# Kernel optimization log

Measured on AMD Instinct MI355X. Metric: run time of the kernel, lower is better.

## Reference

```python
import jax, jax.numpy as jnp
import numpy as np
from jax import lax

TAU = 2.0
NUM_HEADS = 8
EPS = 1e-5
ALPHA = 4.0  # surrogate sigmoid sharpness

@jax.custom_vjp
def heaviside(x):
    # torch.heaviside(x, 1.0): 1 for x >= 0 (value 1 at x==0), 0 for x < 0
    return (x >= 0).astype(x.dtype)

def _hv_fwd(x):
    return (x >= 0).astype(x.dtype), x

def _hv_bwd(x, g):
    s = jax.nn.sigmoid(x * ALPHA)
    return (g * s * (1.0 - s) * ALPHA,)

heaviside.defvjp(_hv_fwd, _hv_bwd)

def lif(x):
    # Leaky-integrate-fire recurrence over leading time axis. x: [T, ...]
    def step(v, xt):
        v = v + (xt - v) / TAU                 # leakage
        s = heaviside(v - 1.0)                 # fire (v_threshold = 1.0)
        v = (1.0 - lax.stop_gradient(s)) * v   # hard reset (detached spike)
        return v, s
    _, spikes = lax.scan(step, jnp.zeros_like(x[0]), x)
    return spikes

def conv1x1(x, w):
    # x: [T,B,Cin,H,W], w: [Cout,Cin] (1x1 conv, no bias)
    return jnp.einsum('tbchw,dc->tbdhw', x, w)

def bn(x, gamma, beta, mean, var):
    # BatchNorm2d in eval mode (running stats), per-channel over axis 2
    shp = (1, 1, -1, 1, 1)
    inv = gamma.reshape(shp) / jnp.sqrt(var.reshape(shp) + EPS)
    return (x - mean.reshape(shp)) * inv + beta.reshape(shp)

def setup_inputs():
    key = jax.random.key(0)
    ks = jax.random.split(key, 10)
    T, B, C, H, W = 4, 32, 256, 16, 16
    Cv = C  # lamda_ratio = 1

    def w_init(k, o, i):
        return jax.random.normal(k, (o, i), jnp.float32) * (1.0 / np.sqrt(i))

    def bn_params(k, c):
        k1, k2, k3, k4 = jax.random.split(k, 4)
        gamma = jax.random.uniform(k1, (c,), jnp.float32, 0.5, 1.5)
        beta = jax.random.normal(k2, (c,), jnp.float32) * 0.1
        mean = jax.random.normal(k3, (c,), jnp.float32) * 0.1
        var = jax.random.uniform(k4, (c,), jnp.float32, 0.5, 1.5)
        return gamma, beta, mean, var

    x = jax.random.normal(ks[0], (T, B, C, H, W), jnp.float32)
    q_w = w_init(ks[1], C, C)
    k_w = w_init(ks[2], C, C)
    v_w = w_init(ks[3], Cv, C)
    proj_w = w_init(ks[4], C, Cv)
    q_gamma, q_beta, q_mean, q_var = bn_params(ks[5], C)
    k_gamma, k_beta, k_mean, k_var = bn_params(ks[6], C)
    v_gamma, v_beta, v_mean, v_var = bn_params(ks[7], Cv)
    p_gamma, p_beta, p_mean, p_var = bn_params(ks[8], C)
    return {
        'x': x,
        'q_w': q_w, 'q_gamma': q_gamma, 'q_beta': q_beta, 'q_mean': q_mean, 'q_var': q_var,
        'k_w': k_w, 'k_gamma': k_gamma, 'k_beta': k_beta, 'k_mean': k_mean, 'k_var': k_var,
        'v_w': v_w, 'v_gamma': v_gamma, 'v_beta': v_beta, 'v_mean': v_mean, 'v_var': v_var,
        'proj_w': proj_w, 'p_gamma': p_gamma, 'p_beta': p_beta, 'p_mean': p_mean, 'p_var': p_var,
    }

def reference(x, q_w, q_gamma, q_beta, q_mean, q_var,
              k_w, k_gamma, k_beta, k_mean, k_var,
              v_w, v_gamma, v_beta, v_mean, v_var,
              proj_w, p_gamma, p_beta, p_mean, p_var):
    T, B, C, H, W = x.shape
    N = H * W
    Cv = v_w.shape[0]
    hd = C // NUM_HEADS
    hdv = Cv // NUM_HEADS
    scale = (C // NUM_HEADS) ** -0.5

    xs = lif(x)  # head_spike

    q = lif(bn(conv1x1(xs, q_w), q_gamma, q_beta, q_mean, q_var))  # [T,B,C,H,W] binary
    k = lif(bn(conv1x1(xs, k_w), k_gamma, k_beta, k_mean, k_var))
    v = lif(bn(conv1x1(xs, v_w), v_gamma, v_beta, v_mean, v_var))  # [T,B,Cv,H,W]

    # channel c = h*hd + d; flatten spatial -> tokens N, split heads
    q = q.reshape(T, B, NUM_HEADS, hd, N).transpose(0, 1, 2, 4, 3)   # [T,B,h,N,d]
    k = k.reshape(T, B, NUM_HEADS, hd, N).transpose(0, 1, 2, 4, 3)
    v = v.reshape(T, B, NUM_HEADS, hdv, N).transpose(0, 1, 2, 4, 3)  # [T,B,h,N,dv]

    attn = jnp.einsum('tbhnd,tbhmd->tbhnm', q, k)                    # QK^T
    out = jnp.einsum('tbhnm,tbhmd->tbhnd', attn, v) * (scale * 2.0)  # (QK^T)V * 2*scale

    out = out.transpose(0, 1, 2, 4, 3).reshape(T, B, Cv, N)          # [T,B,Cv,N]
    out = lif(out)                                                   # attn_spike
    out = out.reshape(T, B, Cv, H, W)
    out = bn(conv1x1(out, proj_w), p_gamma, p_beta, p_mean, p_var)   # [T,B,C,H,W]
    return out
```

## Files before the change

### kernel.cpp

```cpp
#include <hip/hip_runtime.h>

#define TT 4
#define BB 32
#define CC 256
#define NN 256
#define EPSf 1e-5f
#define MULTf 0.35355339059327373f
#define MARGINf 1e-3f
#define FLAG_CAP 524288u

typedef __attribute__((ext_vector_type(8))) short s16x8;
typedef __attribute__((ext_vector_type(4))) float f32x4;
typedef unsigned char uchar;
typedef unsigned int uint;
typedef unsigned short ushort;

__device__ __forceinline__ ushort f2bf_rn(float f) {
  uint u = __float_as_uint(f);
  u = (u + 0x7FFFu + ((u >> 16) & 1u)) >> 16;
  return (ushort)u;
}
__device__ __forceinline__ float bf2f(ushort b) {
  return __uint_as_float(((uint)b) << 16);
}

__device__ __forceinline__ void gload_lds16(const void* g, void* l) {
  __builtin_amdgcn_global_load_lds(
      (const __attribute__((address_space(1))) uint*)g,
      (__attribute__((address_space(3))) uint*)l, 16, 0, 0);
}

__global__ __launch_bounds__(256) void k_lif_frag(const float* __restrict__ x,
                                                  uchar* __restrict__ xsF,
                                                  uchar* __restrict__ xsP) {
#pragma clang fp contract(off)
  const int tid = threadIdx.x;
  const int nt = blockIdx.x;
  const int ks = blockIdx.y;
  const int b = blockIdx.z;
  const int nl = tid & 63;
  const int oct = tid >> 6;
  const int n = nt * 64 + nl;
  const int c0 = ks * 32 + oct * 8;
  const size_t stride = (size_t)BB * CC * NN;
  const float* xb = x + ((size_t)b * CC + c0) * NN + n;

  float v[8];
#pragma unroll
  for (int j = 0; j < 8; ++j) v[j] = 0.f;

#pragma unroll
  for (int t = 0; t < TT; ++t) {
    ushort sp[8];
    uint pm = 0;
#pragma unroll
    for (int j = 0; j < 8; ++j) {
      float xt = xb[t * stride + (size_t)j * NN];
      float d = (xt - v[j]) * 0.5f;
      v[j] = v[j] + d;
      bool s = (v[j] >= 1.0f);
      sp[j] = s ? (ushort)0x3F80 : (ushort)0;
      if (s) { v[j] = 0.f; pm |= 1u << j; }
    }
    uint4* dst = reinterpret_cast<uint4*>(xsF) +
                 (((size_t)(t * BB + b) * 16 + (n >> 4)) * 512 + ks * 64 + oct * 16 + (n & 15));
    uint4 o;
    o.x = (uint)sp[0] | ((uint)sp[1] << 16);
    o.y = (uint)sp[2] | ((uint)sp[3] << 16);
    o.z = (uint)sp[4] | ((uint)sp[5] << 16);
    o.w = (uint)sp[6] | ((uint)sp[7] << 16);
    *dst = o;
    xsP[(((size_t)(t * BB + b) * NN + n) << 5) + ks * 4 + oct] = (uchar)pm;
  }
}

__global__ __launch_bounds__(256) void k_prep_w(
    const float* __restrict__ qw, const float* __restrict__ kw,
    const float* __restrict__ vw, const float* __restrict__ pw,
    uchar* __restrict__ wfq, uchar* __restrict__ wfp,
    uint* __restrict__ flags) {
  const int gid = blockIdx.x * 256 + threadIdx.x;
  if (gid < 4) flags[gid] = 0;
  const int ob2 = gid >> 9;
  const int e = gid & 511;
  const int ks = e >> 6, l = e & 63;
  const float* W;
  uchar* outb;
  int ob_out, nob;
  if (ob2 < 48) {
    const int sel = ob2 >> 4;
    W = sel == 0 ? qw : (sel == 1 ? kw : vw);
    W += ((size_t)((ob2 & 15) * 16 + (l & 15))) * CC;
    outb = wfq; ob_out = ob2; nob = 48;
  } else {
    W = pw + ((size_t)((ob2 - 48) * 16 + (l & 15))) * CC;
    outb = wfp; ob_out = ob2 - 48; nob = 16;
  }
  const int c0 = ks * 32 + (l >> 4) * 8;
  float wv[8];
  *reinterpret_cast<float4*>(&wv[0]) = *reinterpret_cast<const float4*>(W + c0);
  *reinterpret_cast<float4*>(&wv[4]) = *reinterpret_cast<const float4*>(W + c0 + 4);
  ushort hi[8], lo[8];
#pragma unroll
  for (int j = 0; j < 8; ++j) {
    hi[j] = f2bf_rn(wv[j]);
    lo[j] = f2bf_rn(wv[j] - bf2f(hi[j]));
  }
  const size_t base = (((size_t)ob_out * 8 + ks) * 64 + l) * 16;
  const size_t sstr = (size_t)nob * 8 * 64 * 16;
  *reinterpret_cast<uint4*>(outb + base) = *reinterpret_cast<const uint4*>(hi);
  *reinterpret_cast<uint4*>(outb + sstr + base) = *reinterpret_cast<const uint4*>(lo);
}

__global__ __launch_bounds__(256, 2) void k_qkv_mfma(
    const uchar* __restrict__ xsF, const uchar* __restrict__ wfq,
    const float* __restrict__ qga, const float* __restrict__ qbe, const float* __restrict__ qme, const float* __restrict__ qva,
    const float* __restrict__ kga, const float* __restrict__ kbe, const float* __restrict__ kme, const float* __restrict__ kva,
    const float* __restrict__ vga, const float* __restrict__ vbe, const float* __restrict__ vme, const float* __restrict__ vva,
    ushort* __restrict__ qp, uint* __restrict__ flags) {
  __shared__ short lsB[2][4][8][64][8];
  const int tid = threadIdx.x;
  const int w = tid >> 6, lane = tid & 63;
  const int lhi = lane >> 4, llo = lane & 15;
  const int wr = w >> 1, wc = w & 1;
  const int oc0 = blockIdx.x * 64;
  const int ntile = blockIdx.y;
  const int b = blockIdx.z;
  const int sel = oc0 >> 8;
  const float* G  = sel == 0 ? qga : (sel == 1 ? kga : vga);
  const float* Be = sel == 0 ? qbe : (sel == 1 ? kbe : vbe);
  const float* Mn = sel == 0 ? qme : (sel == 1 ? kme : vme);
  const float* Vr = sel == 0 ? qva : (sel == 1 ? kva : vva);

  s16x8 wfr[2][2][8];
#pragma unroll
  for (int s = 0; s < 2; ++s)
#pragma unroll
    for (int mf = 0; mf < 2; ++mf) {
      const int ob = blockIdx.x * 4 + wr * 2 + mf;
#pragma unroll
      for (int ks = 0; ks < 8; ++ks)
        wfr[s][mf][ks] = *reinterpret_cast<const s16x8*>(
            wfq + ((((size_t)s * 48 + ob) * 8 + ks) * 64 + lane) * 16);
    }

  float inv8[2][4], mean8[2][4], beta8[2][4];
#pragma unroll
  for (int mf = 0; mf < 2; ++mf)
#pragma unroll
    for (int r = 0; r < 4; ++r) {
      const int ocb = (oc0 & 255) + wr * 32 + mf * 16 + lhi * 4 + r;
      inv8[mf][r] = G[ocb] / sqrtf(Vr[ocb] + EPSf);
      mean8[mf][r] = Mn[ocb];
      beta8[mf][r] = Be[ocb];
    }

  auto STAGE = [&](int buf, int t) {
    const uchar* src = xsF + (((size_t)(t * BB + b) * 16 + ntile * 4) * 8192);
#pragma unroll
    for (int k2 = 0; k2 < 8; ++k2) {
      const int chunk = w * 8 + k2;
      gload_lds16(src + (size_t)chunk * 1024 + lane * 16,
                  reinterpret_cast<char*>(&lsB[buf][0][0][0][0]) + chunk * 1024);
    }
  };

  float vst[2][2][4];
#pragma unroll
  for (int mf = 0; mf < 2; ++mf)
#pragma unroll
    for (int nf = 0; nf < 2; ++nf)
#pragma unroll
      for (int r = 0; r < 4; ++r) vst[mf][nf][r] = 0.f;
  uint fl = 0;
  ushort qm[TT][4];

  STAGE(0, 0);
  __syncthreads();

#pragma unroll
  for (int t = 0; t < TT; ++t) {
    const int cur = t & 1;
    if (t + 1 < TT) STAGE(cur ^ 1, t + 1);

    f32x4 acc[2][2];
#pragma unroll
    for (int mf = 0; mf < 2; ++mf)
#pragma unroll
      for (int nf = 0; nf < 2; ++nf) acc[mf][nf] = (f32x4){0.f, 0.f, 0.f, 0.f};

#pragma unroll
    for (int ks = 0; ks < 8; ++ks) {
      s16x8 b0 = *reinterpret_cast<const s16x8*>(&lsB[cur][wc * 2][ks][lane][0]);
      s16x8 b1 = *reinterpret_cast<const s16x8*>(&lsB[cur][wc * 2 + 1][ks][lane][0]);
#pragma unroll
      for (int s = 0; s < 2; ++s)
#pragma unroll
        for (int mf = 0; mf < 2; ++mf) {
          acc[mf][0] = __builtin_amdgcn_mfma_f32_16x16x32_bf16(wfr[s][mf][ks], b0, acc[mf][0], 0, 0, 0);
          acc[mf][1] = __builtin_amdgcn_mfma_f32_16x16x32_bf16(wfr[s][mf][ks], b1, acc[mf][1], 0, 0, 0);
        }
    }

#pragma unroll
    for (int mf = 0; mf < 2; ++mf)
#pragma unroll
      for (int nf = 0; nf < 2; ++nf)
#pragma unroll
        for (int r = 0; r < 4; ++r) {
          float y = (acc[mf][nf][r] - mean8[mf][r]) * inv8[mf][r] + beta8[mf][r];
          float v = vst[mf][nf][r];
          v = v + (y - v) * 0.5f;
          const bool sp = (v >= 1.0f);
          if (fabsf(v - 1.0f) < MARGINf) fl |= 1u << ((mf * 2 + nf) * 4 + r);
          const unsigned long long m = __ballot(sp);
          if (llo == r) qm[t][mf * 2 + nf] = (ushort)((m >> (lhi * 16)) & 0xFFFFull);
          vst[mf][nf][r] = sp ? 0.f : v;
        }
    __syncthreads();
  }

  if (llo < 4) {
#pragma unroll
    for (int t = 0; t < TT; ++t) {
      ushort* qrow = qp + (size_t)(t * BB + b) * 768 * 16;
#pragma unroll
      for (int mf = 0; mf < 2; ++mf)
#pragma unroll
        for (int nf = 0; nf < 2; ++nf) {
          const int oc = oc0 + wr * 32 + mf * 16 + lhi * 4 + llo;
          qrow[(size_t)oc * 16 + ntile * 4 + wc * 2 + nf] = qm[t][mf * 2 + nf];
        }
    }
  }

  if (fl) {
    const int cnt = __popc(fl);
    uint base = atomicAdd(flags, (uint)cnt);
#pragma unroll
    for (int mf = 0; mf < 2; ++mf)
#pragma unroll
      for (int nf = 0; nf < 2; ++nf)
#pragma unroll
        for (int r = 0; r < 4; ++r)
          if (fl & (1u << ((mf * 2 + nf) * 4 + r))) {
            const int oc = oc0 + wr * 32 + mf * 16 + lhi * 4 + r;
            const int n = ntile * 64 + wc * 32 + nf * 16 + llo;
            if (base < FLAG_CAP) flags[4 + base] = (((uint)(b << 10) | (uint)oc) << 8) | (uint)n;
            base++;
          }
  }
}

__global__ __launch_bounds__(256) void k_fix(
    const uchar* __restrict__ xsP,
    const float* __restrict__ qw, const float* __restrict__ kw, const float* __restrict__ vw,
    const float* __restrict__ qga, const float* __restrict__ qbe, const float* __restrict__ qme, const float* __restrict__ qva,
    const float* __restrict__ kga, const float* __restrict__ kbe, const float* __restrict__ kme, const float* __restrict__ kva,
    const float* __restrict__ vga, const float* __restrict__ vbe, const float* __restrict__ vme, const float* __restrict__ vva,
    uint* __restrict__ qp32, const uint* __restrict__ flags) {
#pragma clang fp contract(off)
  const uint cnt = min(flags[0], FLAG_CAP);
  for (uint i = blockIdx.x * 256 + threadIdx.x; i < cnt; i += gridDim.x * 256) {
    const uint e = flags[4 + i];
    const int n = e & 255;
    const int oc = (e >> 8) & 1023;
    const int b = e >> 18;
    const int sel = oc >> 8, ocl = oc & 255;
    const float* W = (sel == 0 ? qw : (sel == 1 ? kw : vw)) + (size_t)ocl * CC;
    const float* G  = sel == 0 ? qga : (sel == 1 ? kga : vga);
    const float* Be = sel == 0 ? qbe : (sel == 1 ? kbe : vbe);
    const float* Mn = sel == 0 ? qme : (sel == 1 ? kme : vme);
    const float* Vr = sel == 0 ? qva : (sel == 1 ? kva : vva);

    uint bw[4][8];
#pragma unroll
    for (int t = 0; t < TT; ++t) {
      const uint4* p = reinterpret_cast<const uint4*>(
          xsP + (((size_t)(t * BB + b) * NN + n) << 5));
      uint4 a = p[0], c4 = p[1];
      bw[t][0] = a.x;  bw[t][1] = a.y;  bw[t][2] = a.z;  bw[t][3] = a.w;
      bw[t][4] = c4.x; bw[t][5] = c4.y; bw[t][6] = c4.z; bw[t][7] = c4.w;
    }

    const float4* W4 = reinterpret_cast<const float4*>(W);
    float a0 = 0.f, a1 = 0.f, a2 = 0.f, a3 = 0.f;
#pragma unroll
    for (int g = 0; g < 32; ++g) {
      const float4 w0 = W4[2 * g];
      const float4 w1 = W4[2 * g + 1];
      const uint s0 = bw[0][g >> 2] >> ((g & 3) * 8);
      const uint s1 = bw[1][g >> 2] >> ((g & 3) * 8);
      const uint s2 = bw[2][g >> 2] >> ((g & 3) * 8);
      const uint s3 = bw[3][g >> 2] >> ((g & 3) * 8);
      const float wv[8] = {w0.x, w0.y, w0.z, w0.w, w1.x, w1.y, w1.z, w1.w};
#pragma unroll
      for (int j = 0; j < 8; ++j) {
        a0 = fmaf(wv[j], (float)((s0 >> j) & 1u), a0);
        a1 = fmaf(wv[j], (float)((s1 >> j) & 1u), a1);
        a2 = fmaf(wv[j], (float)((s2 >> j) & 1u), a2);
        a3 = fmaf(wv[j], (float)((s3 >> j) & 1u), a3);
      }
    }
    float accs[4] = {a0, a1, a2, a3};

    const float inv = G[ocl] / sqrtf(Vr[ocl] + EPSf);
    const float mean = Mn[ocl], beta = Be[ocl];
    float v = 0.f;
#pragma unroll
    for (int t = 0; t < TT; ++t) {
      float xm = accs[t] - mean;
      float y = xm * inv;
      y = y + beta;
      float d = (y - v) * 0.5f;
      v = v + d;
      const bool sp = (v >= 1.0f);
      const size_t widx = ((size_t)(t * BB + b) * 768 + oc) * 8 + (n >> 5);
      const uint bit = 1u << (n & 31);
      if (sp) atomicOr(&qp32[widx], bit);
      else atomicAnd(&qp32[widx], ~bit);
      if (sp) v = 0.f;
    }
  }
}

__global__ __launch_bounds__(1024) void k_attn(const ushort* __restrict__ qp,
                                               uchar* __restrict__ attnF) {
  __shared__ uint Qb[32][8], Kb[32][8], Vb[32][8];
  __shared__ int KtV[32][32];
  const int tid = threadIdx.x;
  const int b = blockIdx.x >> 3;
  const int h = blockIdx.x & 7;
  const int n = tid & 255;
  const int jg = tid >> 8;
  const int wordn = n >> 5, bitn = n & 31;

  float vst[8];
#pragma unroll
  for (int j = 0; j < 8; ++j) vst[j] = 0.f;

  for (int t = 0; t < TT; ++t) {
    __syncthreads();
    const ushort* base = qp + (size_t)(t * BB + b) * 768 * 16;
    if (tid < 768) {
      const int arr = tid >> 8;
      const int idx = tid & 255;
      const int ch = idx >> 3, wv2 = idx & 7;
      const uint val = *reinterpret_cast<const uint*>(
          base + (size_t)(arr * 256 + h * 32 + ch) * 16 + wv2 * 2);
      uint(*dst)[8] = (arr == 0) ? Qb : (arr == 1) ? Kb : Vb;
      dst[ch][wv2] = val;
    }
    __syncthreads();
    {
      const int ii = tid >> 5, jj = tid & 31;
      int s = 0;
#pragma unroll
      for (int w8 = 0; w8 < 8; ++w8) s += __popc(Kb[ii][w8] & Vb[jj][w8]);
      KtV[ii][jj] = s;
    }
    __syncthreads();
    int acc[8];
#pragma unroll
    for (int j = 0; j < 8; ++j) acc[j] = 0;
#pragma unroll 4
    for (int ii = 0; ii < 32; ++ii) {
      const int qb = (int)((Qb[ii][wordn] >> bitn) & 1u);
      const int4 k0 = *reinterpret_cast<const int4*>(&KtV[ii][jg * 8]);
      const int4 k1 = *reinterpret_cast<const int4*>(&KtV[ii][jg * 8 + 4]);
      acc[0] += k0.x * qb; acc[1] += k0.y * qb;
      acc[2] += k0.z * qb; acc[3] += k0.w * qb;
      acc[4] += k1.x * qb; acc[5] += k1.y * qb;
      acc[6] += k1.z * qb; acc[7] += k1.w * qb;
    }
    ushort sbit[8];
    {
#pragma clang fp contract(off)
#pragma unroll
      for (int j = 0; j < 8; ++j) {
        float y = (float)acc[j] * MULTf;
        float v = vst[j];
        float d = (y - v) * 0.5f;
        v = v + d;
        const bool sp = (v >= 1.0f);
        sbit[j] = sp ? (ushort)0x3F80 : (ushort)0;
        vst[j] = sp ? 0.f : v;
      }
    }
    uint4 o;
    o.x = (uint)sbit[0] | ((uint)sbit[1] << 16);
    o.y = (uint)sbit[2] | ((uint)sbit[3] << 16);
    o.z = (uint)sbit[4] | ((uint)sbit[5] << 16);
    o.w = (uint)sbit[6] | ((uint)sbit[7] << 16);
    uint4* dst4 = reinterpret_cast<uint4*>(attnF) +
                  (((size_t)(t * BB + b) * 16 + (n >> 4)) * 512 + h * 64 + jg * 16 + (n & 15));
    *dst4 = o;
  }
}

__global__ __launch_bounds__(256, 2) void k_proj_mfma(
    const uchar* __restrict__ attnF, const uchar* __restrict__ wfp,
    const float* __restrict__ pga, const float* __restrict__ pbe,
    const float* __restrict__ pme, const float* __restrict__ pva,
    float* __restrict__ out) {
  __shared__ short lsB[4][8][64][8];
  const int tid = threadIdx.x;
  const int w = tid >> 6, lane = tid & 63;
  const int lhi = lane >> 4, llo = lane & 15;
  const int wr = w >> 1, wc = w & 1;
  const int oc0 = blockIdx.x * 64;
  const int ntile = blockIdx.y;
  const int tb = blockIdx.z;

  s16x8 wfr[2][2][8];
#pragma unroll
  for (int s = 0; s < 2; ++s)
#pragma unroll
    for (int mf = 0; mf < 2; ++mf) {
      const int ob = blockIdx.x * 4 + wr * 2 + mf;
#pragma unroll
      for (int ks = 0; ks < 8; ++ks)
        wfr[s][mf][ks] = *reinterpret_cast<const s16x8*>(
            wfp + ((((size_t)s * 16 + ob) * 8 + ks) * 64 + lane) * 16);
    }

  float inv8[2][4], mean8[2][4], beta8[2][4];
#pragma unroll
  for (int mf = 0; mf < 2; ++mf)
#pragma unroll
    for (int r = 0; r < 4; ++r) {
      const int ocb = oc0 + wr * 32 + mf * 16 + lhi * 4 + r;
      inv8[mf][r] = pga[ocb] / sqrtf(pva[ocb] + EPSf);
      mean8[mf][r] = pme[ocb];
      beta8[mf][r] = pbe[ocb];
    }

  const uchar* src = attnF + (((size_t)tb * 16 + ntile * 4) * 8192);
#pragma unroll
  for (int k2 = 0; k2 < 8; ++k2) {
    const int chunk = w * 8 + k2;
    gload_lds16(src + (size_t)chunk * 1024 + lane * 16,
                reinterpret_cast<char*>(&lsB[0][0][0][0]) + chunk * 1024);
  }
  __syncthreads();

  f32x4 acc[2][2];
#pragma unroll
  for (int mf = 0; mf < 2; ++mf)
#pragma unroll
    for (int nf = 0; nf < 2; ++nf) acc[mf][nf] = (f32x4){0.f, 0.f, 0.f, 0.f};

#pragma unroll
  for (int ks = 0; ks < 8; ++ks) {
    s16x8 b0 = *reinterpret_cast<const s16x8*>(&lsB[wc * 2][ks][lane][0]);
    s16x8 b1 = *reinterpret_cast<const s16x8*>(&lsB[wc * 2 + 1][ks][lane][0]);
#pragma unroll
    for (int s = 0; s < 2; ++s)
#pragma unroll
      for (int mf = 0; mf < 2; ++mf) {
        acc[mf][0] = __builtin_amdgcn_mfma_f32_16x16x32_bf16(wfr[s][mf][ks], b0, acc[mf][0], 0, 0, 0);
        acc[mf][1] = __builtin_amdgcn_mfma_f32_16x16x32_bf16(wfr[s][mf][ks], b1, acc[mf][1], 0, 0, 0);
      }
  }

#pragma unroll
  for (int mf = 0; mf < 2; ++mf)
#pragma unroll
    for (int nf = 0; nf < 2; ++nf)
#pragma unroll
      for (int r = 0; r < 4; ++r) {
        const int oc = oc0 + wr * 32 + mf * 16 + lhi * 4 + r;
        const int nn = ntile * 64 + wc * 32 + nf * 16 + llo;
        float y = (acc[mf][nf][r] - mean8[mf][r]) * inv8[mf][r] + beta8[mf][r];
        out[((size_t)tb * CC + oc) * NN + nn] = y;
      }
}

extern "C" void kernel_launch(void* const* d_in, const int* in_sizes, int n_in,
                              void* d_out, int out_size, void* d_ws, size_t ws_size,
                              hipStream_t stream) {
  const float* x = (const float*)d_in[0];
  const float* q_w = (const float*)d_in[1];
  const float* q_g = (const float*)d_in[2];
  const float* q_b = (const float*)d_in[3];
  const float* q_m = (const float*)d_in[4];
  const float* q_v = (const float*)d_in[5];
  const float* k_w = (const float*)d_in[6];
  const float* k_g = (const float*)d_in[7];
  const float* k_b = (const float*)d_in[8];
  const float* k_m = (const float*)d_in[9];
  const float* k_v = (const float*)d_in[10];
  const float* v_w = (const float*)d_in[11];
  const float* v_g = (const float*)d_in[12];
  const float* v_b = (const float*)d_in[13];
  const float* v_m = (const float*)d_in[14];
  const float* v_v = (const float*)d_in[15];
  const float* p_w = (const float*)d_in[16];
  const float* p_g = (const float*)d_in[17];
  const float* p_b = (const float*)d_in[18];
  const float* p_m = (const float*)d_in[19];
  const float* p_v = (const float*)d_in[20];

  uchar* ws = (uchar*)d_ws;
  uchar* xsF  = ws;
  ushort* qp  = (ushort*)(ws + 16777216);
  uchar* wfq  = ws + 19922944;
  uchar* wfp  = ws + 20709376;
  uint* flags = (uint*)(ws + 20971520);
  uchar* xsP  = ws + 23068672;

  k_prep_w<<<dim3(128), 256, 0, stream>>>(q_w, k_w, v_w, p_w, wfq, wfp, flags);
  k_lif_frag<<<dim3(4, 8, 32), 256, 0, stream>>>(x, xsF, xsP);
  k_qkv_mfma<<<dim3(12, 4, 32), 256, 0, stream>>>(xsF, wfq,
                                                  q_g, q_b, q_m, q_v,
                                                  k_g, k_b, k_m, k_v,
                                                  v_g, v_b, v_m, v_v,
                                                  qp, flags);
  k_fix<<<dim3(64), 256, 0, stream>>>(xsP, q_w, k_w, v_w,
                                      q_g, q_b, q_m, q_v,
                                      k_g, k_b, k_m, k_v,
                                      v_g, v_b, v_m, v_v,
                                      (uint*)qp, flags);
  k_attn<<<dim3(256), 1024, 0, stream>>>(qp, xsF );
  k_proj_mfma<<<dim3(4, 4, 128), 256, 0, stream>>>(xsF, wfp, p_g, p_b, p_m, p_v,
                                                   (float*)d_out);
}
```

Before: 114.1 us.

## Merge front kernels, swap QKV operand staging, and remap blocks across XCDs

```diff
diff --git a/kernel.cpp b/kernel.cpp
--- a/kernel.cpp
+++ b/kernel.cpp
@@ -30,140 +30,129 @@
       (__attribute__((address_space(3))) uint*)l, 16, 0, 0);
 }
 
-__global__ __launch_bounds__(256) void k_lif_frag(const float* __restrict__ x,
-                                                  uchar* __restrict__ xsF,
-                                                  uchar* __restrict__ xsP) {
-#pragma clang fp contract(off)
-  const int tid = threadIdx.x;
-  const int nt = blockIdx.x;
-  const int ks = blockIdx.y;
-  const int b = blockIdx.z;
-  const int nl = tid & 63;
-  const int oct = tid >> 6;
-  const int n = nt * 64 + nl;
-  const int c0 = ks * 32 + oct * 8;
-  const size_t stride = (size_t)BB * CC * NN;
-  const float* xb = x + ((size_t)b * CC + c0) * NN + n;
-
-  float v[8];
-#pragma unroll
-  for (int j = 0; j < 8; ++j) v[j] = 0.f;
-
-#pragma unroll
-  for (int t = 0; t < TT; ++t) {
-    ushort sp[8];
-    uint pm = 0;
-#pragma unroll
-    for (int j = 0; j < 8; ++j) {
-      float xt = xb[t * stride + (size_t)j * NN];
-      float d = (xt - v[j]) * 0.5f;
-      v[j] = v[j] + d;
-      bool s = (v[j] >= 1.0f);
-      sp[j] = s ? (ushort)0x3F80 : (ushort)0;
-      if (s) { v[j] = 0.f; pm |= 1u << j; }
-    }
-    uint4* dst = reinterpret_cast<uint4*>(xsF) +
-                 (((size_t)(t * BB + b) * 16 + (n >> 4)) * 512 + ks * 64 + oct * 16 + (n & 15));
-    uint4 o;
-    o.x = (uint)sp[0] | ((uint)sp[1] << 16);
-    o.y = (uint)sp[2] | ((uint)sp[3] << 16);
-    o.z = (uint)sp[4] | ((uint)sp[5] << 16);
-    o.w = (uint)sp[6] | ((uint)sp[7] << 16);
-    *dst = o;
-    xsP[(((size_t)(t * BB + b) * NN + n) << 5) + ks * 4 + oct] = (uchar)pm;
-  }
-}
-
-__global__ __launch_bounds__(256) void k_prep_w(
+__global__ __launch_bounds__(256) void k_front(
+    const float* __restrict__ x, uchar* __restrict__ xsF, uchar* __restrict__ xsP,
     const float* __restrict__ qw, const float* __restrict__ kw,
     const float* __restrict__ vw, const float* __restrict__ pw,
-    uchar* __restrict__ wfq, uchar* __restrict__ wfp,
-    uint* __restrict__ flags) {
-  const int gid = blockIdx.x * 256 + threadIdx.x;
-  if (gid < 4) flags[gid] = 0;
-  const int ob2 = gid >> 9;
-  const int e = gid & 511;
-  const int ks = e >> 6, l = e & 63;
-  const float* W;
-  uchar* outb;
-  int ob_out, nob;
-  if (ob2 < 48) {
-    const int sel = ob2 >> 4;
-    W = sel == 0 ? qw : (sel == 1 ? kw : vw);
-    W += ((size_t)((ob2 & 15) * 16 + (l & 15))) * CC;
-    outb = wfq; ob_out = ob2; nob = 48;
+    uchar* __restrict__ wfq, uchar* __restrict__ wfp, uint* __restrict__ flags) {
+  const int tid = threadIdx.x;
+  const int bid = blockIdx.x;
+  if (bid < 1024) {
+#pragma clang fp contract(off)
+    const int nt = bid & 3;
+    const int ks = (bid >> 2) & 7;
+    const int b = bid >> 5;
+    const int nl = tid & 63;
+    const int oct = tid >> 6;
+    const int n = nt * 64 + nl;
+    const int c0 = ks * 32 + oct * 8;
+    const size_t stride = (size_t)BB * CC * NN;
+    const float* xb = x + ((size_t)b * CC + c0) * NN + n;
+
+    float v[8];
+#pragma unroll
+    for (int j = 0; j < 8; ++j) v[j] = 0.f;
+
+#pragma unroll
+    for (int t = 0; t < TT; ++t) {
+      ushort sp[8];
+      uint pm = 0;
+#pragma unroll
+      for (int j = 0; j < 8; ++j) {
+        float xt = xb[t * stride + (size_t)j * NN];
+        float d = (xt - v[j]) * 0.5f;
+        v[j] = v[j] + d;
+        bool s = (v[j] >= 1.0f);
+        sp[j] = s ? (ushort)0x3F80 : (ushort)0;
+        if (s) { v[j] = 0.f; pm |= 1u << j; }
+      }
+      uint4* dst = reinterpret_cast<uint4*>(xsF) +
+                   (((size_t)(t * BB + b) * 16 + (n >> 4)) * 512 + ks * 64 + oct * 16 + (n & 15));
+      uint4 o;
+      o.x = (uint)sp[0] | ((uint)sp[1] << 16);
+      o.y = (uint)sp[2] | ((uint)sp[3] << 16);
+      o.z = (uint)sp[4] | ((uint)sp[5] << 16);
+      o.w = (uint)sp[6] | ((uint)sp[7] << 16);
+      *dst = o;
+      xsP[(((size_t)(t * BB + b) * NN + n) << 5) + ks * 4 + oct] = (uchar)pm;
+    }
   } else {
-    W = pw + ((size_t)((ob2 - 48) * 16 + (l & 15))) * CC;
-    outb = wfp; ob_out = ob2 - 48; nob = 16;
-  }
-  const int c0 = ks * 32 + (l >> 4) * 8;
-  float wv[8];
-  *reinterpret_cast<float4*>(&wv[0]) = *reinterpret_cast<const float4*>(W + c0);
-  *reinterpret_cast<float4*>(&wv[4]) = *reinterpret_cast<const float4*>(W + c0 + 4);
-  ushort hi[8], lo[8];
-#pragma unroll
-  for (int j = 0; j < 8; ++j) {
-    hi[j] = f2bf_rn(wv[j]);
-    lo[j] = f2bf_rn(wv[j] - bf2f(hi[j]));
-  }
-  const size_t base = (((size_t)ob_out * 8 + ks) * 64 + l) * 16;
-  const size_t sstr = (size_t)nob * 8 * 64 * 16;
-  *reinterpret_cast<uint4*>(outb + base) = *reinterpret_cast<const uint4*>(hi);
-  *reinterpret_cast<uint4*>(outb + sstr + base) = *reinterpret_cast<const uint4*>(lo);
-}
-
-__global__ __launch_bounds__(256, 2) void k_qkv_mfma(
+    const int gid = (bid - 1024) * 256 + tid;
+    if (gid < 4) flags[gid] = 0;
+    const int ob2 = gid >> 9;
+    const int e = gid & 511;
+    const int ks = e >> 6, l = e & 63;
+    const float* W;
+    uchar* outb;
+    int ob_out, nob;
+    if (ob2 < 48) {
+      const int sel = ob2 >> 4;
+      W = sel == 0 ? qw : (sel == 1 ? kw : vw);
+      W += ((size_t)((ob2 & 15) * 16 + (l & 15))) * CC;
+      outb = wfq; ob_out = ob2; nob = 48;
+    } else {
+      W = pw + ((size_t)((ob2 - 48) * 16 + (l & 15))) * CC;
+      outb = wfp; ob_out = ob2 - 48; nob = 16;
+    }
+    const int c0 = ks * 32 + (l >> 4) * 8;
+    float wv[8];
+    *reinterpret_cast<float4*>(&wv[0]) = *reinterpret_cast<const float4*>(W + c0);
+    *reinterpret_cast<float4*>(&wv[4]) = *reinterpret_cast<const float4*>(W + c0 + 4);
+    ushort hi[8], lo[8];
+#pragma unroll
+    for (int j = 0; j < 8; ++j) {
+      hi[j] = f2bf_rn(wv[j]);
+      lo[j] = f2bf_rn(wv[j] - bf2f(hi[j]));
+    }
+    const size_t base = (((size_t)ob_out * 8 + ks) * 64 + l) * 16;
+    const size_t sstr = (size_t)nob * 8 * 64 * 16;
+    *reinterpret_cast<uint4*>(outb + base) = *reinterpret_cast<const uint4*>(hi);
+    *reinterpret_cast<uint4*>(outb + sstr + base) = *reinterpret_cast<const uint4*>(lo);
+  }
+}
+
+__global__ __launch_bounds__(256) void k_qkv_mfma(
     const uchar* __restrict__ xsF, const uchar* __restrict__ wfq,
     const float* __restrict__ qga, const float* __restrict__ qbe, const float* __restrict__ qme, const float* __restrict__ qva,
     const float* __restrict__ kga, const float* __restrict__ kbe, const float* __restrict__ kme, const float* __restrict__ kva,
     const float* __restrict__ vga, const float* __restrict__ vbe, const float* __restrict__ vme, const float* __restrict__ vva,
     ushort* __restrict__ qp, uint* __restrict__ flags) {
-  __shared__ short lsB[2][4][8][64][8];
+  __shared__ short wlds[64][64][8];
   const int tid = threadIdx.x;
   const int w = tid >> 6, lane = tid & 63;
   const int lhi = lane >> 4, llo = lane & 15;
   const int wr = w >> 1, wc = w & 1;
-  const int oc0 = blockIdx.x * 64;
-  const int ntile = blockIdx.y;
-  const int b = blockIdx.z;
-  const int sel = oc0 >> 8;
+  const int bid = blockIdx.x;
+  const int xcd = bid & 7;
+  const int r = bid >> 3;
+  const int j = r % 12;
+  const int g = (r / 12) * 8 + xcd;
+  const int b = g >> 2, ntile = g & 3;
+  const int oc0 = j * 64;
+  const int sel = j >> 2;
   const float* G  = sel == 0 ? qga : (sel == 1 ? kga : vga);
   const float* Be = sel == 0 ? qbe : (sel == 1 ? kbe : vbe);
   const float* Mn = sel == 0 ? qme : (sel == 1 ? kme : vme);
   const float* Vr = sel == 0 ? qva : (sel == 1 ? kva : vva);
 
-  s16x8 wfr[2][2][8];
-#pragma unroll
-  for (int s = 0; s < 2; ++s)
-#pragma unroll
-    for (int mf = 0; mf < 2; ++mf) {
-      const int ob = blockIdx.x * 4 + wr * 2 + mf;
-#pragma unroll
-      for (int ks = 0; ks < 8; ++ks)
-        wfr[s][mf][ks] = *reinterpret_cast<const s16x8*>(
-            wfq + ((((size_t)s * 48 + ob) * 8 + ks) * 64 + lane) * 16);
-    }
+#pragma unroll
+  for (int i = 0; i < 16; ++i) {
+    const int cg = w * 16 + i;
+    const int s = cg >> 5, rem = cg & 31, obl = rem >> 3, ks = rem & 7;
+    const size_t gsrc = ((((size_t)s * 48 + j * 4 + obl) * 8 + ks) * 64 + lane) * 16;
+    gload_lds16(wfq + gsrc, reinterpret_cast<char*>(&wlds[0][0][0]) + cg * 1024);
+  }
 
   float inv8[2][4], mean8[2][4], beta8[2][4];
 #pragma unroll
   for (int mf = 0; mf < 2; ++mf)
 #pragma unroll
-    for (int r = 0; r < 4; ++r) {
-      const int ocb = (oc0 & 255) + wr * 32 + mf * 16 + lhi * 4 + r;
-      inv8[mf][r] = G[ocb] / sqrtf(Vr[ocb] + EPSf);
-      mean8[mf][r] = Mn[ocb];
-      beta8[mf][r] = Be[ocb];
-    }
-
-  auto STAGE = [&](int buf, int t) {
-    const uchar* src = xsF + (((size_t)(t * BB + b) * 16 + ntile * 4) * 8192);
-#pragma unroll
-    for (int k2 = 0; k2 < 8; ++k2) {
-      const int chunk = w * 8 + k2;
-      gload_lds16(src + (size_t)chunk * 1024 + lane * 16,
-                  reinterpret_cast<char*>(&lsB[buf][0][0][0][0]) + chunk * 1024);
-    }
-  };
+    for (int rr = 0; rr < 4; ++rr) {
+      const int ocb = (oc0 & 255) + wr * 32 + mf * 16 + lhi * 4 + rr;
+      inv8[mf][rr] = G[ocb] / sqrtf(Vr[ocb] + EPSf);
+      mean8[mf][rr] = Mn[ocb];
+      beta8[mf][rr] = Be[ocb];
+    }
 
   float vst[2][2][4];
 #pragma unroll
@@ -171,54 +160,67 @@
 #pragma unroll
     for (int nf = 0; nf < 2; ++nf)
 #pragma unroll
-      for (int r = 0; r < 4; ++r) vst[mf][nf][r] = 0.f;
+      for (int rr = 0; rr < 4; ++rr) vst[mf][nf][rr] = 0.f;
   uint fl = 0;
   ushort qm[TT][4];
 
-  STAGE(0, 0);
+  const int nb0 = ntile * 4 + wc * 2;
   __syncthreads();
 
-#pragma unroll
-  for (int t = 0; t < TT; ++t) {
-    const int cur = t & 1;
-    if (t + 1 < TT) STAGE(cur ^ 1, t + 1);
-
-    f32x4 acc[2][2];
-#pragma unroll
-    for (int mf = 0; mf < 2; ++mf)
-#pragma unroll
-      for (int nf = 0; nf < 2; ++nf) acc[mf][nf] = (f32x4){0.f, 0.f, 0.f, 0.f};
-
-#pragma unroll
-    for (int ks = 0; ks < 8; ++ks) {
-      s16x8 b0 = *reinterpret_cast<const s16x8*>(&lsB[cur][wc * 2][ks][lane][0]);
-      s16x8 b1 = *reinterpret_cast<const s16x8*>(&lsB[cur][wc * 2 + 1][ks][lane][0]);
-#pragma unroll
-      for (int s = 0; s < 2; ++s)
-#pragma unroll
-        for (int mf = 0; mf < 2; ++mf) {
-          acc[mf][0] = __builtin_amdgcn_mfma_f32_16x16x32_bf16(wfr[s][mf][ks], b0, acc[mf][0], 0, 0, 0);
-          acc[mf][1] = __builtin_amdgcn_mfma_f32_16x16x32_bf16(wfr[s][mf][ks], b1, acc[mf][1], 0, 0, 0);
-        }
-    }
-
-#pragma unroll
-    for (int mf = 0; mf < 2; ++mf)
-#pragma unroll
-      for (int nf = 0; nf < 2; ++nf)
-#pragma unroll
-        for (int r = 0; r < 4; ++r) {
-          float y = (acc[mf][nf][r] - mean8[mf][r]) * inv8[mf][r] + beta8[mf][r];
-          float v = vst[mf][nf][r];
-          v = v + (y - v) * 0.5f;
-          const bool sp = (v >= 1.0f);
-          if (fabsf(v - 1.0f) < MARGINf) fl |= 1u << ((mf * 2 + nf) * 4 + r);
-          const unsigned long long m = __ballot(sp);
-          if (llo == r) qm[t][mf * 2 + nf] = (ushort)((m >> (lhi * 16)) & 0xFFFFull);
-          vst[mf][nf][r] = sp ? 0.f : v;
-        }
-    __syncthreads();
-  }
+#define BPTR(t_, nb_, ks_)                                              \
+  reinterpret_cast<const s16x8*>(                                       \
+      xsF + ((((size_t)((t_) * BB + b) * 16 + (nb_)) * 512 + (ks_) * 64 + lane) * 16))
+
+  s16x8 bA[2][8], bB[2][8];
+#pragma unroll
+  for (int ks = 0; ks < 8; ++ks) {
+    bA[0][ks] = *BPTR(0, nb0, ks);
+    bA[1][ks] = *BPTR(0, nb0 + 1, ks);
+  }
+
+#define QKV_STEP(t_, CUR, NXT, PRE)                                             \
+  {                                                                             \
+    if (PRE) {                                                                  \
+      _Pragma("unroll") for (int ks = 0; ks < 8; ++ks) {                        \
+        NXT[0][ks] = *BPTR((t_) + 1, nb0, ks);                                  \
+        NXT[1][ks] = *BPTR((t_) + 1, nb0 + 1, ks);                              \
+      }                                                                         \
+    }                                                                           \
+    f32x4 acc[2][2];                                                            \
+    _Pragma("unroll") for (int mf = 0; mf < 2; ++mf)                            \
+        _Pragma("unroll") for (int nf = 0; nf < 2; ++nf)                        \
+            acc[mf][nf] = (f32x4){0.f, 0.f, 0.f, 0.f};                          \
+    _Pragma("unroll") for (int ks = 0; ks < 8; ++ks) {                          \
+      _Pragma("unroll") for (int s = 0; s < 2; ++s)                             \
+          _Pragma("unroll") for (int mf = 0; mf < 2; ++mf) {                    \
+        s16x8 wf = *reinterpret_cast<const s16x8*>(                             \
+            &wlds[s * 32 + (wr * 2 + mf) * 8 + ks][lane][0]);                   \
+        acc[mf][0] = __builtin_amdgcn_mfma_f32_16x16x32_bf16(wf, CUR[0][ks],    \
+                                                             acc[mf][0], 0, 0, 0); \
+        acc[mf][1] = __builtin_amdgcn_mfma_f32_16x16x32_bf16(wf, CUR[1][ks],    \
+                                                             acc[mf][1], 0, 0, 0); \
+      }                                                                         \
+    }                                                                           \
+    _Pragma("unroll") for (int mf = 0; mf < 2; ++mf)                            \
+        _Pragma("unroll") for (int nf = 0; nf < 2; ++nf)                        \
+            _Pragma("unroll") for (int rr = 0; rr < 4; ++rr) {                  \
+      float y = (acc[mf][nf][rr] - mean8[mf][rr]) * inv8[mf][rr] + beta8[mf][rr]; \
+      float v = vst[mf][nf][rr];                                                \
+      v = v + (y - v) * 0.5f;                                                   \
+      const bool sp = (v >= 1.0f);                                              \
+      if (fabsf(v - 1.0f) < MARGINf) fl |= 1u << ((mf * 2 + nf) * 4 + rr);      \
+      const unsigned long long m = __ballot(sp);                                \
+      if (llo == rr) qm[t_][mf * 2 + nf] = (ushort)((m >> (lhi * 16)) & 0xFFFFull); \
+      vst[mf][nf][rr] = sp ? 0.f : v;                                           \
+    }                                                                           \
+  }
+
+  QKV_STEP(0, bA, bB, 1)
+  QKV_STEP(1, bB, bA, 1)
+  QKV_STEP(2, bA, bB, 1)
+  QKV_STEP(3, bB, bA, 0)
+#undef QKV_STEP
+#undef BPTR
 
   if (llo < 4) {
 #pragma unroll
@@ -242,9 +244,9 @@
 #pragma unroll
       for (int nf = 0; nf < 2; ++nf)
 #pragma unroll
-        for (int r = 0; r < 4; ++r)
-          if (fl & (1u << ((mf * 2 + nf) * 4 + r))) {
-            const int oc = oc0 + wr * 32 + mf * 16 + lhi * 4 + r;
+        for (int rr = 0; rr < 4; ++rr)
+          if (fl & (1u << ((mf * 2 + nf) * 4 + rr))) {
+            const int oc = oc0 + wr * 32 + mf * 16 + lhi * 4 + rr;
             const int n = ntile * 64 + wc * 32 + nf * 16 + llo;
             if (base < FLAG_CAP) flags[4 + base] = (((uint)(b << 10) | (uint)oc) << 8) | (uint)n;
             base++;
@@ -295,11 +297,11 @@
       const uint s3 = bw[3][g >> 2] >> ((g & 3) * 8);
       const float wv[8] = {w0.x, w0.y, w0.z, w0.w, w1.x, w1.y, w1.z, w1.w};
 #pragma unroll
-      for (int j = 0; j < 8; ++j) {
-        a0 = fmaf(wv[j], (float)((s0 >> j) & 1u), a0);
-        a1 = fmaf(wv[j], (float)((s1 >> j) & 1u), a1);
-        a2 = fmaf(wv[j], (float)((s2 >> j) & 1u), a2);
-        a3 = fmaf(wv[j], (float)((s3 >> j) & 1u), a3);
+      for (int jj = 0; jj < 8; ++jj) {
+        a0 = fmaf(wv[jj], (float)((s0 >> jj) & 1u), a0);
+        a1 = fmaf(wv[jj], (float)((s1 >> jj) & 1u), a1);
+        a2 = fmaf(wv[jj], (float)((s2 >> jj) & 1u), a2);
+        a3 = fmaf(wv[jj], (float)((s3 >> jj) & 1u), a3);
       }
     }
     float accs[4] = {a0, a1, a2, a3};
@@ -398,51 +400,55 @@
   }
 }
 
-__global__ __launch_bounds__(256, 2) void k_proj_mfma(
+__global__ __launch_bounds__(256) void k_proj_mfma(
     const uchar* __restrict__ attnF, const uchar* __restrict__ wfp,
     const float* __restrict__ pga, const float* __restrict__ pbe,
     const float* __restrict__ pme, const float* __restrict__ pva,
     float* __restrict__ out) {
-  __shared__ short lsB[4][8][64][8];
   const int tid = threadIdx.x;
   const int w = tid >> 6, lane = tid & 63;
   const int lhi = lane >> 4, llo = lane & 15;
   const int wr = w >> 1, wc = w & 1;
-  const int oc0 = blockIdx.x * 64;
-  const int ntile = blockIdx.y;
-  const int tb = blockIdx.z;
+  const int bid = blockIdx.x;
+  const int xcd = bid & 7;
+  const int r = bid >> 3;
+  const int j = r & 3;
+  const int g = (r >> 2) * 8 + xcd;
+  const int tb = g >> 2, ntile = g & 3;
+  const int oc0 = j * 64;
 
   s16x8 wfr[2][2][8];
 #pragma unroll
   for (int s = 0; s < 2; ++s)
 #pragma unroll
     for (int mf = 0; mf < 2; ++mf) {
-      const int ob = blockIdx.x * 4 + wr * 2 + mf;
+      const int ob = j * 4 + wr * 2 + mf;
 #pragma unroll
       for (int ks = 0; ks < 8; ++ks)
         wfr[s][mf][ks] = *reinterpret_cast<const s16x8*>(
             wfp + ((((size_t)s * 16 + ob) * 8 + ks) * 64 + lane) * 16);
     }
 
+  const int nb0 = ntile * 4 + wc * 2;
+  s16x8 bfr[2][8];
+#pragma unroll
+  for (int ks = 0; ks < 8; ++ks) {
+    bfr[0][ks] = *reinterpret_cast<const s16x8*>(
+        attnF + ((((size_t)tb * 16 + nb0) * 512 + ks * 64 + lane) * 16));
+    bfr[1][ks] = *reinterpret_cast<const s16x8*>(
+        attnF + ((((size_t)tb * 16 + nb0 + 1) * 512 + ks * 64 + lane) * 16));
+  }
+
   float inv8[2][4], mean8[2][4], beta8[2][4];
 #pragma unroll
   for (int mf = 0; mf < 2; ++mf)
 #pragma unroll
-    for (int r = 0; r < 4; ++r) {
-      const int ocb = oc0 + wr * 32 + mf * 16 + lhi * 4 + r;
-      inv8[mf][r] = pga[ocb] / sqrtf(pva[ocb] + EPSf);
-      mean8[mf][r] = pme[ocb];
-      beta8[mf][r] = pbe[ocb];
-    }
-
-  const uchar* src = attnF + (((size_t)tb * 16 + ntile * 4) * 8192);
-#pragma unroll
-  for (int k2 = 0; k2 < 8; ++k2) {
-    const int chunk = w * 8 + k2;
-    gload_lds16(src + (size_t)chunk * 1024 + lane * 16,
-                reinterpret_cast<char*>(&lsB[0][0][0][0]) + chunk * 1024);
-  }
-  __syncthreads();
+    for (int rr = 0; rr < 4; ++rr) {
+      const int ocb = oc0 + wr * 32 + mf * 16 + lhi * 4 + rr;
+      inv8[mf][rr] = pga[ocb] / sqrtf(pva[ocb] + EPSf);
+      mean8[mf][rr] = pme[ocb];
+      beta8[mf][rr] = pbe[ocb];
+    }
 
   f32x4 acc[2][2];
 #pragma unroll
@@ -452,14 +458,12 @@
 
 #pragma unroll
   for (int ks = 0; ks < 8; ++ks) {
-    s16x8 b0 = *reinterpret_cast<const s16x8*>(&lsB[wc * 2][ks][lane][0]);
-    s16x8 b1 = *reinterpret_cast<const s16x8*>(&lsB[wc * 2 + 1][ks][lane][0]);
 #pragma unroll
     for (int s = 0; s < 2; ++s)
 #pragma unroll
       for (int mf = 0; mf < 2; ++mf) {
-        acc[mf][0] = __builtin_amdgcn_mfma_f32_16x16x32_bf16(wfr[s][mf][ks], b0, acc[mf][0], 0, 0, 0);
-        acc[mf][1] = __builtin_amdgcn_mfma_f32_16x16x32_bf16(wfr[s][mf][ks], b1, acc[mf][1], 0, 0, 0);
+        acc[mf][0] = __builtin_amdgcn_mfma_f32_16x16x32_bf16(wfr[s][mf][ks], bfr[0][ks], acc[mf][0], 0, 0, 0);
+        acc[mf][1] = __builtin_amdgcn_mfma_f32_16x16x32_bf16(wfr[s][mf][ks], bfr[1][ks], acc[mf][1], 0, 0, 0);
       }
   }
 
@@ -468,10 +472,10 @@
 #pragma unroll
     for (int nf = 0; nf < 2; ++nf)
 #pragma unroll
-      for (int r = 0; r < 4; ++r) {
-        const int oc = oc0 + wr * 32 + mf * 16 + lhi * 4 + r;
+      for (int rr = 0; rr < 4; ++rr) {
+        const int oc = oc0 + wr * 32 + mf * 16 + lhi * 4 + rr;
         const int nn = ntile * 64 + wc * 32 + nf * 16 + llo;
-        float y = (acc[mf][nf][r] - mean8[mf][r]) * inv8[mf][r] + beta8[mf][r];
+        float y = (acc[mf][nf][rr] - mean8[mf][rr]) * inv8[mf][rr] + beta8[mf][rr];
         out[((size_t)tb * CC + oc) * NN + nn] = y;
       }
 }
@@ -509,19 +513,19 @@
   uint* flags = (uint*)(ws + 20971520);
   uchar* xsP  = ws + 23068672;
 
-  k_prep_w<<<dim3(128), 256, 0, stream>>>(q_w, k_w, v_w, p_w, wfq, wfp, flags);
-  k_lif_frag<<<dim3(4, 8, 32), 256, 0, stream>>>(x, xsF, xsP);
-  k_qkv_mfma<<<dim3(12, 4, 32), 256, 0, stream>>>(xsF, wfq,
-                                                  q_g, q_b, q_m, q_v,
-                                                  k_g, k_b, k_m, k_v,
-                                                  v_g, v_b, v_m, v_v,
-                                                  qp, flags);
+  k_front<<<dim3(1152), 256, 0, stream>>>(x, xsF, xsP, q_w, k_w, v_w, p_w,
+                                          wfq, wfp, flags);
+  k_qkv_mfma<<<dim3(1536), 256, 0, stream>>>(xsF, wfq,
+                                             q_g, q_b, q_m, q_v,
+                                             k_g, k_b, k_m, k_v,
+                                             v_g, v_b, v_m, v_v,
+                                             qp, flags);
   k_fix<<<dim3(64), 256, 0, stream>>>(xsP, q_w, k_w, v_w,
                                       q_g, q_b, q_m, q_v,
                                       k_g, k_b, k_m, k_v,
                                       v_g, v_b, v_m, v_v,
                                       (uint*)qp, flags);
   k_attn<<<dim3(256), 1024, 0, stream>>>(qp, xsF );
-  k_proj_mfma<<<dim3(4, 4, 128), 256, 0, stream>>>(xsF, wfp, p_g, p_b, p_m, p_v,
-                                                   (float*)d_out);
-}
+  k_proj_mfma<<<dim3(2048), 256, 0, stream>>>(xsF, wfp, p_g, p_b, p_m, p_v,
+                                              (float*)d_out);
+}
```

Result: no change. 112.3 us (-1.6%).
